# Kernel optimization log

Hardware: AMD Instinct MI355X
Metric: run time of the kernel (lower is better)

The kernel has to match this reference:

```python
import jax, jax.numpy as jnp
import numpy as np

D_MODEL = 192
D_STATE = 16
D_CONV = 3
EXPAND = 2
D_INNER = EXPAND * D_MODEL
DT_RANK = (D_MODEL + 15) // 16  # ceil(d_model/16) = 12


def setup_inputs() -> dict:
    key = jax.random.key(0)
    ks = jax.random.split(key, 8)
    B, H, W = 4, 32, 32
    sc = lambda n: 1.0 / np.sqrt(n)
    x = jax.random.normal(ks[0], (B, H, W, D_MODEL), jnp.float32)
    W_in = jax.random.normal(ks[1], (D_MODEL, 2 * D_INNER), jnp.float32) * sc(D_MODEL)
    conv_w = jax.random.normal(ks[2], (D_INNER, 1, D_CONV, D_CONV), jnp.float32) * sc(D_CONV * D_CONV)
    conv_b = jnp.zeros((D_INNER,), jnp.float32)
    W_x = jax.random.normal(ks[3], (D_INNER, DT_RANK + 2 * D_STATE), jnp.float32) * sc(D_INNER)
    W_dt = jax.random.normal(ks[4], (DT_RANK, D_INNER), jnp.float32) * sc(DT_RANK)
    b_dt = jnp.zeros((D_INNER,), jnp.float32)
    A_log = jnp.log(jnp.tile(jnp.arange(1, D_STATE + 1, dtype=jnp.float32), (D_INNER, 1)))
    D_param = jnp.ones((D_INNER,), jnp.float32)
    W_out = jax.random.normal(ks[5], (D_INNER, D_MODEL), jnp.float32) * sc(D_INNER)
    gamma = jnp.ones((D_INNER,), jnp.float32)
    beta = jnp.zeros((D_INNER,), jnp.float32)
    return {"x": x, "W_in": W_in, "conv_w": conv_w, "conv_b": conv_b,
            "W_x": W_x, "W_dt": W_dt, "b_dt": b_dt, "A_log": A_log,
            "D_param": D_param, "W_out": W_out, "gamma": gamma, "beta": beta}


def _ssm_scan(u, W_x, W_dt, b_dt, A_log, D_param):
    # u: (B, L, D_inner). Log-cumsum closed-form linear SSM scan.
    x_dbl = u @ W_x                                   # (B,L,dt_rank+2N)
    dt = x_dbl[..., :DT_RANK]
    B_mat = x_dbl[..., DT_RANK:DT_RANK + D_STATE]     # (B,L,N)
    C_mat = x_dbl[..., DT_RANK + D_STATE:]            # (B,L,N)
    dt = jax.nn.softplus(dt @ W_dt + b_dt)            # (B,L,D)
    A = -jnp.exp(A_log)                               # (D,N)
    log_dA = jnp.einsum('bld,dn->bldn', dt, A)        # (B,L,D,N)
    dB_u = jnp.einsum('bld,bln->bldn', dt, B_mat) * u[..., None]
    log_decay = jnp.cumsum(log_dA, axis=1)
    decay = jnp.exp(log_decay)
    h = decay * jnp.cumsum(dB_u / (decay + 1e-12), axis=1)
    y = jnp.einsum('bldn,bln->bld', h, C_mat)
    return y + u * D_param


def reference(x, W_in, conv_w, conv_b, W_x, W_dt, b_dt, A_log, D_param, W_out, gamma, beta):
    B, H, W, C = x.shape
    xz = x @ W_in                                     # (B,H,W,2*D_inner)
    x_val, z = xz[..., :D_INNER], xz[..., D_INNER:]
    # depthwise 3x3 conv in NCHW
    xc = jnp.transpose(x_val, (0, 3, 1, 2))
    xc = jax.lax.conv_general_dilated(
        xc, conv_w, window_strides=(1, 1), padding='SAME',
        feature_group_count=D_INNER,
        dimension_numbers=('NCHW', 'OIHW', 'NCHW'))
    xc = xc + conv_b[None, :, None, None]
    xc = jax.nn.silu(xc)
    xv = jnp.transpose(xc, (0, 2, 3, 1))              # (B,H,W,D_inner)

    scan = lambda u: _ssm_scan(u, W_x, W_dt, b_dt, A_log, D_param)
    s1 = xv.reshape(B, H * W, D_INNER)                # row-major
    s2 = s1[:, ::-1]
    s3 = jnp.transpose(xv, (0, 2, 1, 3)).reshape(B, W * H, D_INNER)  # column-major
    s4 = s3[:, ::-1]
    y1 = scan(s1)
    y2 = scan(s2)[:, ::-1]
    y3 = scan(s3)
    y4 = scan(s4)[:, ::-1]
    # map column-major scans back to row-major order
    y3 = jnp.transpose(y3.reshape(B, W, H, D_INNER), (0, 2, 1, 3)).reshape(B, H * W, D_INNER)
    y4 = jnp.transpose(y4.reshape(B, W, H, D_INNER), (0, 2, 1, 3)).reshape(B, H * W, D_INNER)
    y = y1 + y2 + y3 + y4

    # LayerNorm over last dim (eps=1e-5)
    mu = jnp.mean(y, axis=-1, keepdims=True)
    var = jnp.mean(jnp.square(y - mu), axis=-1, keepdims=True)
    y = (y - mu) * jax.lax.rsqrt(var + 1e-5) * gamma + beta

    y = y.reshape(B, H, W, D_INNER) * jax.nn.silu(z)
    return y @ W_out
```

## Files before the change

kernel.cpp:

```cpp
#include <hip/hip_runtime.h>
#include <hip/hip_fp16.h>

#define DMODEL 192
#define DINNER 384
#define NPOS   4096
#define SEQL   1024
#define DSTATE 16
#define DTRANK 12
#define TILE   32

__device__ __forceinline__ float silu_f(float v) { return v * (1.f / (1.f + __expf(-v))); }

__device__ __forceinline__ int scan_pos(int dir, int l) {
    int s = (dir & 1) ? (SEQL - 1 - l) : l;
    return (dir & 2) ? (((s & 31) << 5) | (s >> 5)) : s;
}

template<int CTRL>
__device__ __forceinline__ float dpp_mov(float v) {
    return __int_as_float(__builtin_amdgcn_update_dpp(
        0, __float_as_int(v), CTRL, 0xF, 0xF, true));
}

__global__ void k1_inproj(const float* __restrict__ x, const float* __restrict__ W_in,
                          float* __restrict__ x_val, float* __restrict__ gz) {
    const int t = threadIdx.x;
    const int bi = blockIdx.x;
    const int colg = bi % 3;
    const int pos0 = (bi / 3) << 3;
    const int col = colg * 256 + t;

    const float* xr = x + pos0 * DMODEL;

    float acc[8] = {0,0,0,0,0,0,0,0};
    for (int c = 0; c < DMODEL; c += 4) {
        float w0 = W_in[(c + 0) * 768 + col];
        float w1 = W_in[(c + 1) * 768 + col];
        float w2 = W_in[(c + 2) * 768 + col];
        float w3 = W_in[(c + 3) * 768 + col];
#pragma unroll
        for (int g = 0; g < 8; ++g) {
            const float4 xv = *(const float4*)&xr[g * DMODEL + c];
            acc[g] += xv.x * w0 + xv.y * w1 + xv.z * w2 + xv.w * w3;
        }
    }
    if (col < DINNER) {
#pragma unroll
        for (int g = 0; g < 8; ++g) x_val[(pos0 + g) * DINNER + col] = acc[g];
    } else {
#pragma unroll
        for (int g = 0; g < 8; ++g) gz[(pos0 + g) * DINNER + (col - DINNER)] = silu_f(acc[g]);
    }
}

__global__ void k2_conv_dt(const float* __restrict__ x_val,
                           const float* __restrict__ conv_w, const float* __restrict__ conv_b,
                           const float* __restrict__ W_x, const float* __restrict__ W_dt,
                           const float* __restrict__ b_dt, const float* __restrict__ Dp,
                           __half* __restrict__ u_out, float* __restrict__ xd_out,
                           float* __restrict__ dt32, float* __restrict__ y_acc) {
    __shared__ float us[DINNER];
    __shared__ float part[8 * 44];
    __shared__ float xdl[44];
    const int t = threadIdx.x;
    const int pos = blockIdx.x;
    const int b = pos >> 10, hw = pos & 1023, h = hw >> 5, w = hw & 31;

    float acc = conv_b[t];
#pragma unroll
    for (int i = 0; i < 3; ++i) {
        int hh = h + i - 1;
        if (hh < 0 || hh > 31) continue;
#pragma unroll
        for (int j = 0; j < 3; ++j) {
            int ww = w + j - 1;
            if (ww < 0 || ww > 31) continue;
            acc += x_val[((b * 32 + hh) * 32 + ww) * DINNER + t] * conv_w[t * 9 + i * 3 + j];
        }
    }
    float uv = silu_f(acc);
    us[t] = uv;
    u_out[pos * DINNER + t] = __float2half(uv);
    __syncthreads();

    if (t < 352) {
        int o = t % 44, p = t / 44;
        float s = 0.f;
        int j0 = p * 48;
        for (int j = j0; j < j0 + 48; ++j) s += us[j] * W_x[j * 44 + o];
        part[p * 44 + o] = s;
    }
    __syncthreads();
    if (t < 44) {
        float s = 0.f;
#pragma unroll
        for (int p = 0; p < 8; ++p) s += part[p * 44 + t];
        int o;
        if (t < DTRANK)               o = t;
        else if (t < DTRANK + DSTATE) o = DTRANK + 2 * (t - DTRANK);
        else                          o = DTRANK + 1 + 2 * (t - DTRANK - DSTATE);
        xd_out[pos * 48 + o] = s;
        xdl[t] = s;
    }
    __syncthreads();

    float raw = b_dt[t];
#pragma unroll
    for (int r = 0; r < DTRANK; ++r) raw += xdl[r] * W_dt[r * DINNER + t];
    dt32[pos * DINNER + t] = fmaxf(raw, 0.f) + log1pf(__expf(-fabsf(raw)));

    y_acc[pos * DINNER + t] = 4.f * Dp[t] * uv;
}

__device__ __forceinline__ void gll16(const void* g, void* l) {
    __builtin_amdgcn_global_load_lds(
        (const __attribute__((address_space(1))) void*)g,
        (__attribute__((address_space(3))) void*)l, 16, 0, 0);
}

__device__ __forceinline__ void k3_stage(int l0, int dir, int d0, int wv, int lane,
                                         const float* __restrict__ dtb,
                                         const float* __restrict__ xb,
                                         const __half* __restrict__ ub,
                                         float* dt_d, float* bc_d, __half* u_d) {
    if (wv == 0) {
#pragma unroll
        for (int s = 0; s < 2; ++s) {
            int j = s * 16 + (lane >> 2);
            int pos = scan_pos(dir, l0 + j);
            gll16(dtb + pos * DINNER + d0 + (lane & 3) * 4, dt_d + s * 16 * 16);
        }
    } else if (wv == 3) {
        int pos = scan_pos(dir, l0 + (lane >> 1));
        gll16((const char*)ub + (size_t)(pos * DINNER + d0) * 2 + (lane & 1) * 16, u_d);
    } else {
        int jb0 = (wv - 1) * 16;
#pragma unroll
        for (int s = 0; s < 2; ++s) {
            int jb = jb0 + s * 8;
            int pos = scan_pos(dir, l0 + jb + (lane >> 3));
            gll16(xb + pos * 48 + DTRANK + (lane & 7) * 4, bc_d + jb * 32);
        }
    }
}

__device__ __forceinline__ bool k3_chunk(float A, float& cum, float& S,
                                         const float* __restrict__ dt_s,
                                         const float* __restrict__ bc_s,
                                         const __half* __restrict__ u_s,
                                         int jb, int l0, int dir, int dl, int n,
                                         float* __restrict__ yb, int d) {
    float dtv[8], Bv[8], Cv[8], uv[8];
#pragma unroll
    for (int k = 0; k < 8; ++k) {
        dtv[k] = dt_s[(jb + k) * 16 + dl];
        Bv[k]  = bc_s[(jb + k) * 32 + 2 * n];
        Cv[k]  = bc_s[(jb + k) * 32 + 2 * n + 1];
        uv[k]  = __half2float(u_s[(jb + k) * 16 + dl]);
    }
    float decay[8];
#pragma unroll
    for (int k = 0; k < 8; ++k) { cum += dtv[k] * A; decay[k] = __builtin_amdgcn_exp2f(cum); }
    float rc[8];
#pragma unroll
    for (int k = 0; k < 8; ++k) rc[k] = __builtin_amdgcn_rcpf(decay[k] + 1e-12f);
    float c[8];
#pragma unroll
    for (int k = 0; k < 8; ++k) {
        S += (dtv[k] * Bv[k] * uv[k]) * rc[k];
        c[k] = decay[k] * S * Cv[k];
    }
#pragma unroll
    for (int k = 0; k < 8; ++k) {
        float v = c[k];
        v += dpp_mov<0xB1>(v);
        v += dpp_mov<0x4E>(v);
        v += dpp_mov<0x124>(v);
        v += dpp_mov<0x128>(v);
        c[k] = v;
    }
    if (n == 0) {
#pragma unroll
        for (int k = 0; k < 8; ++k) {
            int pos = scan_pos(dir, l0 + jb + k);
            atomicAdd(&yb[pos * DINNER + d], c[k]);
        }
    }
    return __ballot(cum > -158.7f) != 0ull;
}

__global__ void __launch_bounds__(256, 1)
k3_scan(const __half* __restrict__ u, const float* __restrict__ xd,
        const float* __restrict__ dt32, const float* __restrict__ A_log,
        float* __restrict__ y_acc) {
    __shared__ float  dt_s[2][TILE * 16];
    __shared__ float  BC_s[2][TILE * 32];
    __shared__ __half u_s [2][TILE * 16];
    __shared__ int    alive_w[2][4];

    const int t = threadIdx.x;
    const int lane = t & 63, wv = t >> 6;
    const int n = t & 15, dl = t >> 4;
    const int bi = blockIdx.x;
    const int chunk = bi % 24;
    const int b = (bi / 24) % 4;
    const int dir = bi / 96;
    const int d0 = chunk * 16, d = d0 + dl;

    const float A = -__expf(A_log[d * DSTATE + n]) * 1.4426950408889634f;

    const __half* ub  = u    + b * SEQL * DINNER;
    const float* xb   = xd   + b * SEQL * 48;
    const float* dtb  = dt32 + b * SEQL * DINNER;
    float* yb = y_acc + b * SEQL * DINNER;

    k3_stage(0, dir, d0, wv, lane, dtb, xb, ub, dt_s[0], BC_s[0], u_s[0]);
    __syncthreads();

    float cum = 0.f, S = 0.f;
    bool alive = true;
    int buf = 0, par = 0;
    for (int l0 = 0; l0 < SEQL; l0 += TILE) {
        const int ln = (l0 + TILE < SEQL) ? (l0 + TILE) : l0;
        k3_stage(ln, dir, d0, wv, lane, dtb, xb, ub,
                 dt_s[buf ^ 1], BC_s[buf ^ 1], u_s[buf ^ 1]);
        if (alive) {
#pragma unroll
            for (int jb = 0; jb < TILE; jb += 8) {
                alive = k3_chunk(A, cum, S, dt_s[buf], BC_s[buf], u_s[buf],
                                 jb, l0, dir, dl, n, yb, d);
                if (!alive) break;
            }
        }
        if (lane == 0) alive_w[par][wv] = alive ? 1 : 0;
        __syncthreads();
        const int any = alive_w[par][0] | alive_w[par][1] | alive_w[par][2] | alive_w[par][3];
        buf ^= 1; par ^= 1;
        if (!any) return;
    }
}

__global__ void k4_out(const float* __restrict__ y_acc, const float* __restrict__ gz,
                       const float* __restrict__ gamma, const float* __restrict__ beta,
                       const float* __restrict__ W_out, float* __restrict__ out) {
    __shared__ float g_s[8 * DINNER];
    __shared__ float red[12];
    const int t = threadIdx.x;
    const int half = t / 192, tc = t % 192;
    const int lane = t & 63, wv = t >> 6;
    const int pos0 = blockIdx.x << 3;

    const float g0c = gamma[tc], g1c = gamma[tc + 192];
    const float b0c = beta[tc],  b1c = beta[tc + 192];

    for (int it = 0; it < 4; ++it) {
        int p = it * 2 + half;
        int pos = pos0 + p;
        float y0 = y_acc[pos * DINNER + tc];
        float y1 = y_acc[pos * DINNER + tc + 192];

        float s = y0 + y1;
#pragma unroll
        for (int off = 32; off > 0; off >>= 1) s += __shfl_xor(s, off);
        if (lane == 0) red[wv] = s;
        __syncthreads();
        float mu = (red[half * 3] + red[half * 3 + 1] + red[half * 3 + 2]) * (1.f / 384.f);

        float d0 = y0 - mu, d1 = y1 - mu;
        float sq = d0 * d0 + d1 * d1;
#pragma unroll
        for (int off = 32; off > 0; off >>= 1) sq += __shfl_xor(sq, off);
        if (lane == 0) red[6 + wv] = sq;
        __syncthreads();
        float var = (red[6 + half * 3] + red[6 + half * 3 + 1] + red[6 + half * 3 + 2]) * (1.f / 384.f);
        float inv = rsqrtf(var + 1e-5f);

        g_s[p * DINNER + tc]       = (d0 * inv * g0c + b0c) * gz[pos * DINNER + tc];
        g_s[p * DINNER + tc + 192] = (d1 * inv * g1c + b1c) * gz[pos * DINNER + tc + 192];
    }
    __syncthreads();

    float acc[4] = {0.f, 0.f, 0.f, 0.f};
    const int pbase = half * 4;
    for (int dd = 0; dd < DINNER; dd += 4) {
        float w0 = W_out[(dd + 0) * DMODEL + tc];
        float w1 = W_out[(dd + 1) * DMODEL + tc];
        float w2 = W_out[(dd + 2) * DMODEL + tc];
        float w3 = W_out[(dd + 3) * DMODEL + tc];
#pragma unroll
        for (int i = 0; i < 4; ++i) {
            const float4 g = *(const float4*)&g_s[(pbase + i) * DINNER + dd];
            acc[i] += g.x * w0 + g.y * w1 + g.z * w2 + g.w * w3;
        }
    }
#pragma unroll
    for (int i = 0; i < 4; ++i) out[(pos0 + pbase + i) * DMODEL + tc] = acc[i];
}

extern "C" void kernel_launch(void* const* d_in, const int* in_sizes, int n_in,
                              void* d_out, int out_size, void* d_ws, size_t ws_size,
                              hipStream_t stream) {
    (void)in_sizes; (void)n_in; (void)out_size; (void)ws_size;
    const float* x      = (const float*)d_in[0];
    const float* W_in   = (const float*)d_in[1];
    const float* conv_w = (const float*)d_in[2];
    const float* conv_b = (const float*)d_in[3];
    const float* W_x    = (const float*)d_in[4];
    const float* W_dt   = (const float*)d_in[5];
    const float* b_dt   = (const float*)d_in[6];
    const float* A_log  = (const float*)d_in[7];
    const float* Dp     = (const float*)d_in[8];
    const float* W_out  = (const float*)d_in[9];
    const float* gamma  = (const float*)d_in[10];
    const float* beta   = (const float*)d_in[11];

    char* base = (char*)d_ws;
    float*  x_val = (float*)base;
    __half* u     = (__half*)(base + 6291456);
    float*  xd    = (float*)(base + 9437184);
    float*  dt32  = (float*)(base + 10223616);
    float*  gz    = (float*)(base + 16515072);
    float*  y_acc = (float*)(base + 22806528);

    hipLaunchKernelGGL(k1_inproj, dim3(NPOS / 8 * 3), dim3(256), 0, stream, x, W_in, x_val, gz);
    hipLaunchKernelGGL(k2_conv_dt, dim3(NPOS), dim3(384), 0, stream,
                       x_val, conv_w, conv_b, W_x, W_dt, b_dt, Dp, u, xd, dt32, y_acc);
    hipLaunchKernelGGL(k3_scan, dim3(384), dim3(256), 0, stream,
                       u, xd, dt32, A_log, y_acc);
    hipLaunchKernelGGL(k4_out, dim3(NPOS / 8), dim3(384), 0, stream,
                       y_acc, gz, gamma, beta, W_out, (float*)d_out);
}
```

Before: 203.7 us.

## Split SSM scan into segmented three-pass chunked scan across more blocks

The sequential scan over 1024 positions per (dir,batch,channel-chunk) block is replaced by three kernels. The first computes per-32-step dt partial sums. The second computes each 128-step segment's local state contribution. The third combines prefix decay and prior segment states, then rescans its segment to emit outputs. This raises the block count from 384 to 3072 to fill the GPU and shorten the serial critical path. The cost is two extra launches, extra global traffic, and each segment being scanned twice.

```diff
diff --git a/kernel.cpp b/kernel.cpp
--- a/kernel.cpp
+++ b/kernel.cpp
@@ -8,6 +8,9 @@
 #define DSTATE 16
 #define DTRANK 12
 #define TILE   32
+#define NSEG   8
+#define SEGL   128
+#define NFINE  32
 
 __device__ __forceinline__ float silu_f(float v) { return v * (1.f / (1.f + __expf(-v))); }
 
@@ -189,54 +192,177 @@
     return __ballot(cum > -158.7f) != 0ull;
 }
 
+__global__ void k3a_dtsum(const float* __restrict__ dt32, float* __restrict__ dtsum) {
+    const int t = threadIdx.x;
+    const int bi = blockIdx.x;
+    const int f = bi & 31;
+    const int b = (bi >> 5) & 3;
+    const int ord = bi >> 7;
+    const float* dtb = dt32 + b * SEQL * DINNER;
+    float s = 0.f;
+#pragma unroll 4
+    for (int j = 0; j < 32; ++j) {
+        int sidx = f * 32 + j;
+        int pos = ord ? (((sidx & 31) << 5) | (sidx >> 5)) : sidx;
+        s += dtb[pos * DINNER + t];
+    }
+    dtsum[((ord * 4 + b) * NFINE + f) * DINNER + t] = s;
+}
+
+__device__ __forceinline__ float k3_cum_in(const float* __restrict__ dtsum,
+                                           int dir, int b, int g, int d, float A) {
+    const float* dts = dtsum + ((dir >> 1) * 4 + b) * NFINE * DINNER;
+    float p0 = 0.f, p1 = 0.f, p2 = 0.f, p3 = 0.f;
+    const int fpmax = 4 * g;
+    for (int fp = 0; fp < fpmax; fp += 4) {
+        int h0 = (dir & 1) ? (NFINE - 1 - (fp + 0)) : (fp + 0);
+        int h1 = (dir & 1) ? (NFINE - 1 - (fp + 1)) : (fp + 1);
+        int h2 = (dir & 1) ? (NFINE - 1 - (fp + 2)) : (fp + 2);
+        int h3 = (dir & 1) ? (NFINE - 1 - (fp + 3)) : (fp + 3);
+        p0 += dts[h0 * DINNER + d];
+        p1 += dts[h1 * DINNER + d];
+        p2 += dts[h2 * DINNER + d];
+        p3 += dts[h3 * DINNER + d];
+    }
+    return A * ((p0 + p1) + (p2 + p3));
+}
+
 __global__ void __launch_bounds__(256, 1)
-k3_scan(const __half* __restrict__ u, const float* __restrict__ xd,
+k3b_sseg(const __half* __restrict__ u, const float* __restrict__ xd,
+         const float* __restrict__ dt32, const float* __restrict__ A_log,
+         const float* __restrict__ dtsum, float* __restrict__ S_seg) {
+    __shared__ float  dt_s[2][TILE * 16];
+    __shared__ float  BC_s[2][TILE * 32];
+    __shared__ __half u_s [2][TILE * 16];
+    __shared__ int    vote[4];
+
+    const int t = threadIdx.x;
+    const int lane = t & 63, wv = t >> 6;
+    const int n = t & 15, dl = t >> 4;
+    const int bi = blockIdx.x;
+    const int g = bi & 7;
+    const int r = bi >> 3;
+    const int chunk = r % 24;
+    const int r2 = r / 24;
+    const int b = r2 & 3, dir = r2 >> 2;
+    const int d0 = chunk * 16, d = d0 + dl;
+
+    const float A = -__expf(A_log[d * DSTATE + n]) * 1.4426950408889634f;
+    float cum = k3_cum_in(dtsum, dir, b, g, d, A);
+
+    bool alive = (__ballot(cum > -158.7f) != 0ull);
+    if (lane == 0) vote[wv] = alive ? 1 : 0;
+    __syncthreads();
+    float* Sout = S_seg + bi * 256 + t;
+    if (!(vote[0] | vote[1] | vote[2] | vote[3])) { *Sout = 0.f; return; }
+
+    const __half* ub  = u    + b * SEQL * DINNER;
+    const float* xb   = xd   + b * SEQL * 48;
+    const float* dtb  = dt32 + b * SEQL * DINNER;
+
+    const int l0 = g * SEGL;
+    k3_stage(l0, dir, d0, wv, lane, dtb, xb, ub, dt_s[0], BC_s[0], u_s[0]);
+    __syncthreads();
+
+    float S = 0.f;
+    int buf = 0;
+    for (int tt = 0; tt < SEGL / TILE; ++tt) {
+        const int lc = l0 + tt * TILE;
+        const int ln = (tt < SEGL / TILE - 1) ? (lc + TILE) : lc;
+        k3_stage(ln, dir, d0, wv, lane, dtb, xb, ub,
+                 dt_s[buf ^ 1], BC_s[buf ^ 1], u_s[buf ^ 1]);
+        if (alive) {
+#pragma unroll
+            for (int jb = 0; jb < TILE; jb += 8) {
+                float dtv[8], Bv[8], uv[8];
+#pragma unroll
+                for (int k = 0; k < 8; ++k) {
+                    dtv[k] = dt_s[buf][(jb + k) * 16 + dl];
+                    Bv[k]  = BC_s[buf][(jb + k) * 32 + 2 * n];
+                    uv[k]  = __half2float(u_s[buf][(jb + k) * 16 + dl]);
+                }
+                float decay[8];
+#pragma unroll
+                for (int k = 0; k < 8; ++k) { cum += dtv[k] * A; decay[k] = __builtin_amdgcn_exp2f(cum); }
+                float rc[8];
+#pragma unroll
+                for (int k = 0; k < 8; ++k) rc[k] = __builtin_amdgcn_rcpf(decay[k] + 1e-12f);
+#pragma unroll
+                for (int k = 0; k < 8; ++k) S += (dtv[k] * Bv[k] * uv[k]) * rc[k];
+                alive = (__ballot(cum > -158.7f) != 0ull);
+                if (!alive) break;
+            }
+        }
+        __syncthreads();
+        buf ^= 1;
+    }
+    *Sout = S;
+}
+
+__global__ void __launch_bounds__(256, 1)
+k3c_out(const __half* __restrict__ u, const float* __restrict__ xd,
         const float* __restrict__ dt32, const float* __restrict__ A_log,
+        const float* __restrict__ dtsum, const float* __restrict__ S_seg,
         float* __restrict__ y_acc) {
     __shared__ float  dt_s[2][TILE * 16];
     __shared__ float  BC_s[2][TILE * 32];
     __shared__ __half u_s [2][TILE * 16];
-    __shared__ int    alive_w[2][4];
+    __shared__ int    vote[4];
 
     const int t = threadIdx.x;
     const int lane = t & 63, wv = t >> 6;
     const int n = t & 15, dl = t >> 4;
     const int bi = blockIdx.x;
-    const int chunk = bi % 24;
-    const int b = (bi / 24) % 4;
-    const int dir = bi / 96;
+    const int g = bi & 7;
+    const int r = bi >> 3;
+    const int chunk = r % 24;
+    const int r2 = r / 24;
+    const int b = r2 & 3, dir = r2 >> 2;
     const int d0 = chunk * 16, d = d0 + dl;
 
     const float A = -__expf(A_log[d * DSTATE + n]) * 1.4426950408889634f;
+    float cum = k3_cum_in(dtsum, dir, b, g, d, A);
+
+    bool alive = (__ballot(cum > -158.7f) != 0ull);
+    if (lane == 0) vote[wv] = alive ? 1 : 0;
+    __syncthreads();
+    if (!(vote[0] | vote[1] | vote[2] | vote[3])) return;
+
+    float S;
+    {
+        const float* Sp = S_seg + (size_t)(bi - g) * 256 + t;
+        float s0 = 0.f, s1 = 0.f;
+        int gp = 0;
+        for (; gp + 1 < g; gp += 2) { s0 += Sp[gp * 256]; s1 += Sp[(gp + 1) * 256]; }
+        if (gp < g) s0 += Sp[gp * 256];
+        S = s0 + s1;
+    }
 
     const __half* ub  = u    + b * SEQL * DINNER;
     const float* xb   = xd   + b * SEQL * 48;
     const float* dtb  = dt32 + b * SEQL * DINNER;
     float* yb = y_acc + b * SEQL * DINNER;
 
-    k3_stage(0, dir, d0, wv, lane, dtb, xb, ub, dt_s[0], BC_s[0], u_s[0]);
-    __syncthreads();
-
-    float cum = 0.f, S = 0.f;
-    bool alive = true;
-    int buf = 0, par = 0;
-    for (int l0 = 0; l0 < SEQL; l0 += TILE) {
-        const int ln = (l0 + TILE < SEQL) ? (l0 + TILE) : l0;
+    const int l0 = g * SEGL;
+    k3_stage(l0, dir, d0, wv, lane, dtb, xb, ub, dt_s[0], BC_s[0], u_s[0]);
+    __syncthreads();
+
+    int buf = 0;
+    for (int tt = 0; tt < SEGL / TILE; ++tt) {
+        const int lc = l0 + tt * TILE;
+        const int ln = (tt < SEGL / TILE - 1) ? (lc + TILE) : lc;
         k3_stage(ln, dir, d0, wv, lane, dtb, xb, ub,
                  dt_s[buf ^ 1], BC_s[buf ^ 1], u_s[buf ^ 1]);
         if (alive) {
 #pragma unroll
             for (int jb = 0; jb < TILE; jb += 8) {
                 alive = k3_chunk(A, cum, S, dt_s[buf], BC_s[buf], u_s[buf],
-                                 jb, l0, dir, dl, n, yb, d);
+                                 jb, lc, dir, dl, n, yb, d);
                 if (!alive) break;
             }
         }
-        if (lane == 0) alive_w[par][wv] = alive ? 1 : 0;
         __syncthreads();
-        const int any = alive_w[par][0] | alive_w[par][1] | alive_w[par][2] | alive_w[par][3];
-        buf ^= 1; par ^= 1;
-        if (!any) return;
+        buf ^= 1;
     }
 }
 
@@ -321,12 +447,17 @@
     float*  dt32  = (float*)(base + 10223616);
     float*  gz    = (float*)(base + 16515072);
     float*  y_acc = (float*)(base + 22806528);
+    float*  dtsum = (float*)(base + 29097984);
+    float*  S_seg = (float*)(base + 29491200);
 
     hipLaunchKernelGGL(k1_inproj, dim3(NPOS / 8 * 3), dim3(256), 0, stream, x, W_in, x_val, gz);
     hipLaunchKernelGGL(k2_conv_dt, dim3(NPOS), dim3(384), 0, stream,
                        x_val, conv_w, conv_b, W_x, W_dt, b_dt, Dp, u, xd, dt32, y_acc);
-    hipLaunchKernelGGL(k3_scan, dim3(384), dim3(256), 0, stream,
-                       u, xd, dt32, A_log, y_acc);
+    hipLaunchKernelGGL(k3a_dtsum, dim3(256), dim3(384), 0, stream, dt32, dtsum);
+    hipLaunchKernelGGL(k3b_sseg, dim3(4 * 4 * 24 * NSEG), dim3(256), 0, stream,
+                       u, xd, dt32, A_log, dtsum, S_seg);
+    hipLaunchKernelGGL(k3c_out, dim3(4 * 4 * 24 * NSEG), dim3(256), 0, stream,
+                       u, xd, dt32, A_log, dtsum, S_seg, y_acc);
     hipLaunchKernelGGL(k4_out, dim3(NPOS / 8), dim3(384), 0, stream,
                        y_acc, gz, gamma, beta, W_out, (float*)d_out);
 }
```

New measurement: 283.6 us. 1.39x slower.

## Process two channel groups per scan thread to halve scan blocks and share B/C loads

Applied to the files above, without the earlier changes.

The scan kernel now assigns 32 channels per block instead of 16, so each thread runs two independent recurrences (A and B) interleaved, with single-channel fallbacks once one of them dies out. B/C staging is shared across twice as many channels, and the two chains give more instruction-level parallelism. The grid shrinks from 384 to 192 blocks. This lowers occupancy and parallelism on a chip with many CUs, and raises register pressure.

```diff
diff --git a/kernel.cpp b/kernel.cpp
--- a/kernel.cpp
+++ b/kernel.cpp
@@ -125,14 +125,17 @@
                                          float* dt_d, float* bc_d, __half* u_d) {
     if (wv == 0) {
 #pragma unroll
+        for (int s = 0; s < 4; ++s) {
+            int pos = scan_pos(dir, l0 + s * 8 + (lane >> 3));
+            gll16(dtb + pos * DINNER + d0 + (lane & 7) * 4, dt_d + s * 8 * 32);
+        }
+    } else if (wv == 3) {
+#pragma unroll
         for (int s = 0; s < 2; ++s) {
-            int j = s * 16 + (lane >> 2);
-            int pos = scan_pos(dir, l0 + j);
-            gll16(dtb + pos * DINNER + d0 + (lane & 3) * 4, dt_d + s * 16 * 16);
-        }
-    } else if (wv == 3) {
-        int pos = scan_pos(dir, l0 + (lane >> 1));
-        gll16((const char*)ub + (size_t)(pos * DINNER + d0) * 2 + (lane & 1) * 16, u_d);
+            int pos = scan_pos(dir, l0 + s * 16 + (lane >> 2));
+            gll16((const char*)ub + (size_t)(pos * DINNER + d0) * 2 + (lane & 3) * 16,
+                  u_d + s * 16 * 32);
+        }
     } else {
         int jb0 = (wv - 1) * 16;
 #pragma unroll
@@ -144,19 +147,20 @@
     }
 }
 
-__device__ __forceinline__ bool k3_chunk(float A, float& cum, float& S,
-                                         const float* __restrict__ dt_s,
-                                         const float* __restrict__ bc_s,
-                                         const __half* __restrict__ u_s,
-                                         int jb, int l0, int dir, int dl, int n,
-                                         float* __restrict__ yb, int d) {
+__device__ __forceinline__ bool k3_chunk1(float A, float& cum, float& S,
+                                          const float* __restrict__ dt_s,
+                                          const float* __restrict__ bc_s,
+                                          const __half* __restrict__ u_s,
+                                          int jb, int l0, int dir, int dl, int n,
+                                          float* __restrict__ yb, int d, int coff) {
     float dtv[8], Bv[8], Cv[8], uv[8];
 #pragma unroll
     for (int k = 0; k < 8; ++k) {
-        dtv[k] = dt_s[(jb + k) * 16 + dl];
-        Bv[k]  = bc_s[(jb + k) * 32 + 2 * n];
-        Cv[k]  = bc_s[(jb + k) * 32 + 2 * n + 1];
-        uv[k]  = __half2float(u_s[(jb + k) * 16 + dl]);
+        int row = (jb + k) * 32;
+        dtv[k] = dt_s[row + coff + dl];
+        Bv[k]  = bc_s[row + 2 * n];
+        Cv[k]  = bc_s[row + 2 * n + 1];
+        uv[k]  = __half2float(u_s[row + coff + dl]);
     }
     float decay[8];
 #pragma unroll
@@ -189,25 +193,87 @@
     return __ballot(cum > -158.7f) != 0ull;
 }
 
+__device__ __forceinline__ void k3_chunk2(float AA, float AB,
+                                          float& cumA, float& cumB,
+                                          float& SA, float& SB,
+                                          const float* __restrict__ dt_s,
+                                          const float* __restrict__ bc_s,
+                                          const __half* __restrict__ u_s,
+                                          int jb, int l0, int dir, int dl, int n,
+                                          float* __restrict__ yb, int d0,
+                                          bool& aliveA, bool& aliveB) {
+    float dtvA[8], dtvB[8], Bv[8], Cv[8], uvA[8], uvB[8];
+#pragma unroll
+    for (int k = 0; k < 8; ++k) {
+        int row = (jb + k) * 32;
+        dtvA[k] = dt_s[row + dl];
+        dtvB[k] = dt_s[row + 16 + dl];
+        Bv[k]   = bc_s[row + 2 * n];
+        Cv[k]   = bc_s[row + 2 * n + 1];
+        uvA[k]  = __half2float(u_s[row + dl]);
+        uvB[k]  = __half2float(u_s[row + 16 + dl]);
+    }
+    float decA[8], decB[8];
+#pragma unroll
+    for (int k = 0; k < 8; ++k) {
+        cumA += dtvA[k] * AA; decA[k] = __builtin_amdgcn_exp2f(cumA);
+        cumB += dtvB[k] * AB; decB[k] = __builtin_amdgcn_exp2f(cumB);
+    }
+    float rcA[8], rcB[8];
+#pragma unroll
+    for (int k = 0; k < 8; ++k) {
+        rcA[k] = __builtin_amdgcn_rcpf(decA[k] + 1e-12f);
+        rcB[k] = __builtin_amdgcn_rcpf(decB[k] + 1e-12f);
+    }
+    float cA[8], cB[8];
+#pragma unroll
+    for (int k = 0; k < 8; ++k) {
+        SA += (dtvA[k] * Bv[k] * uvA[k]) * rcA[k];
+        cA[k] = decA[k] * SA * Cv[k];
+        SB += (dtvB[k] * Bv[k] * uvB[k]) * rcB[k];
+        cB[k] = decB[k] * SB * Cv[k];
+    }
+#pragma unroll
+    for (int k = 0; k < 8; ++k) {
+        float vA = cA[k], vB = cB[k];
+        vA += dpp_mov<0xB1>(vA);   vB += dpp_mov<0xB1>(vB);
+        vA += dpp_mov<0x4E>(vA);   vB += dpp_mov<0x4E>(vB);
+        vA += dpp_mov<0x124>(vA);  vB += dpp_mov<0x124>(vB);
+        vA += dpp_mov<0x128>(vA);  vB += dpp_mov<0x128>(vB);
+        cA[k] = vA; cB[k] = vB;
+    }
+    if (n == 0) {
+#pragma unroll
+        for (int k = 0; k < 8; ++k) {
+            int pos = scan_pos(dir, l0 + jb + k);
+            atomicAdd(&yb[pos * DINNER + d0 + dl], cA[k]);
+            atomicAdd(&yb[pos * DINNER + d0 + 16 + dl], cB[k]);
+        }
+    }
+    aliveA = __ballot(cumA > -158.7f) != 0ull;
+    aliveB = __ballot(cumB > -158.7f) != 0ull;
+}
+
 __global__ void __launch_bounds__(256, 1)
 k3_scan(const __half* __restrict__ u, const float* __restrict__ xd,
         const float* __restrict__ dt32, const float* __restrict__ A_log,
         float* __restrict__ y_acc) {
-    __shared__ float  dt_s[2][TILE * 16];
+    __shared__ float  dt_s[2][TILE * 32];
     __shared__ float  BC_s[2][TILE * 32];
-    __shared__ __half u_s [2][TILE * 16];
+    __shared__ __half u_s [2][TILE * 32];
     __shared__ int    alive_w[2][4];
 
     const int t = threadIdx.x;
     const int lane = t & 63, wv = t >> 6;
     const int n = t & 15, dl = t >> 4;
     const int bi = blockIdx.x;
-    const int chunk = bi % 24;
-    const int b = (bi / 24) % 4;
-    const int dir = bi / 96;
-    const int d0 = chunk * 16, d = d0 + dl;
-
-    const float A = -__expf(A_log[d * DSTATE + n]) * 1.4426950408889634f;
+    const int cp = bi % 12;
+    const int b = (bi / 12) % 4;
+    const int dir = bi / 48;
+    const int d0 = cp * 32;
+
+    const float AA = -__expf(A_log[(d0 + dl) * DSTATE + n])      * 1.4426950408889634f;
+    const float AB = -__expf(A_log[(d0 + 16 + dl) * DSTATE + n]) * 1.4426950408889634f;
 
     const __half* ub  = u    + b * SEQL * DINNER;
     const float* xb   = xd   + b * SEQL * 48;
@@ -217,22 +283,31 @@
     k3_stage(0, dir, d0, wv, lane, dtb, xb, ub, dt_s[0], BC_s[0], u_s[0]);
     __syncthreads();
 
-    float cum = 0.f, S = 0.f;
-    bool alive = true;
+    float cumA = 0.f, SA = 0.f, cumB = 0.f, SB = 0.f;
+    bool aliveA = true, aliveB = true;
     int buf = 0, par = 0;
     for (int l0 = 0; l0 < SEQL; l0 += TILE) {
         const int ln = (l0 + TILE < SEQL) ? (l0 + TILE) : l0;
         k3_stage(ln, dir, d0, wv, lane, dtb, xb, ub,
                  dt_s[buf ^ 1], BC_s[buf ^ 1], u_s[buf ^ 1]);
-        if (alive) {
+        if (aliveA | aliveB) {
 #pragma unroll
             for (int jb = 0; jb < TILE; jb += 8) {
-                alive = k3_chunk(A, cum, S, dt_s[buf], BC_s[buf], u_s[buf],
-                                 jb, l0, dir, dl, n, yb, d);
-                if (!alive) break;
+                if (aliveA & aliveB) {
+                    k3_chunk2(AA, AB, cumA, cumB, SA, SB,
+                              dt_s[buf], BC_s[buf], u_s[buf],
+                              jb, l0, dir, dl, n, yb, d0, aliveA, aliveB);
+                } else if (aliveA) {
+                    aliveA = k3_chunk1(AA, cumA, SA, dt_s[buf], BC_s[buf], u_s[buf],
+                                       jb, l0, dir, dl, n, yb, d0 + dl, 0);
+                } else {
+                    aliveB = k3_chunk1(AB, cumB, SB, dt_s[buf], BC_s[buf], u_s[buf],
+                                       jb, l0, dir, dl, n, yb, d0 + 16 + dl, 16);
+                }
+                if (!(aliveA | aliveB)) break;
             }
         }
-        if (lane == 0) alive_w[par][wv] = alive ? 1 : 0;
+        if (lane == 0) alive_w[par][wv] = (aliveA | aliveB) ? 1 : 0;
         __syncthreads();
         const int any = alive_w[par][0] | alive_w[par][1] | alive_w[par][2] | alive_w[par][3];
         buf ^= 1; par ^= 1;
@@ -325,7 +400,7 @@
     hipLaunchKernelGGL(k1_inproj, dim3(NPOS / 8 * 3), dim3(256), 0, stream, x, W_in, x_val, gz);
     hipLaunchKernelGGL(k2_conv_dt, dim3(NPOS), dim3(384), 0, stream,
                        x_val, conv_w, conv_b, W_x, W_dt, b_dt, Dp, u, xd, dt32, y_acc);
-    hipLaunchKernelGGL(k3_scan, dim3(384), dim3(256), 0, stream,
+    hipLaunchKernelGGL(k3_scan, dim3(192), dim3(256), 0, stream,
                        u, xd, dt32, A_log, y_acc);
     hipLaunchKernelGGL(k4_out, dim3(NPOS / 8), dim3(384), 0, stream,
                        y_acc, gz, gamma, beta, W_out, (float*)d_out);
```

Result: slower. 215.4 us (+5.8%).

## Split scan sequence into four parallel segments with two-pass carry propagation

Applied to the files above, without the earlier changes.

The sequential scan over 1024 positions is split into four 256-long segments, each handled by 256 threads of a 1024-thread block. A first lean pass computes each segment's partial dB*u/decay sum, and per-segment dt prefix sums give the starting log-decay. A second pass then recomputes the outputs with the carried-in state. This shortens the serial dependency chain by about four times, at the cost of roughly double the arithmetic, extra LDS use and block-wide syncs.

```diff
diff --git a/kernel.cpp b/kernel.cpp
--- a/kernel.cpp
+++ b/kernel.cpp
@@ -8,6 +8,8 @@
 #define DSTATE 16
 #define DTRANK 12
 #define TILE   32
+#define NSEG   4
+#define SEGL   256
 
 __device__ __forceinline__ float silu_f(float v) { return v * (1.f / (1.f + __expf(-v))); }
 
@@ -118,23 +120,23 @@
         (__attribute__((address_space(3))) void*)l, 16, 0, 0);
 }
 
-__device__ __forceinline__ void k3_stage(int l0, int dir, int d0, int wv, int lane,
+__device__ __forceinline__ void k3_stage(int l0, int dir, int d0, int wrole, int lane,
                                          const float* __restrict__ dtb,
                                          const float* __restrict__ xb,
                                          const __half* __restrict__ ub,
                                          float* dt_d, float* bc_d, __half* u_d) {
-    if (wv == 0) {
+    if (wrole == 0) {
 #pragma unroll
         for (int s = 0; s < 2; ++s) {
             int j = s * 16 + (lane >> 2);
             int pos = scan_pos(dir, l0 + j);
             gll16(dtb + pos * DINNER + d0 + (lane & 3) * 4, dt_d + s * 16 * 16);
         }
-    } else if (wv == 3) {
+    } else if (wrole == 3) {
         int pos = scan_pos(dir, l0 + (lane >> 1));
         gll16((const char*)ub + (size_t)(pos * DINNER + d0) * 2 + (lane & 1) * 16, u_d);
     } else {
-        int jb0 = (wv - 1) * 16;
+        int jb0 = (wrole - 1) * 16;
 #pragma unroll
         for (int s = 0; s < 2; ++s) {
             int jb = jb0 + s * 8;
@@ -142,6 +144,29 @@
             gll16(xb + pos * 48 + DTRANK + (lane & 7) * 4, bc_d + jb * 32);
         }
     }
+}
+
+__device__ __forceinline__ bool k3_chunk_lean(float A, float& cum, float& S,
+                                              const float* __restrict__ dt_s,
+                                              const float* __restrict__ bc_s,
+                                              const __half* __restrict__ u_s,
+                                              int jb, int dl, int n) {
+    float dtv[8], Bv[8], uv[8];
+#pragma unroll
+    for (int k = 0; k < 8; ++k) {
+        dtv[k] = dt_s[(jb + k) * 16 + dl];
+        Bv[k]  = bc_s[(jb + k) * 32 + 2 * n];
+        uv[k]  = __half2float(u_s[(jb + k) * 16 + dl]);
+    }
+    float decay[8];
+#pragma unroll
+    for (int k = 0; k < 8; ++k) { cum += dtv[k] * A; decay[k] = __builtin_amdgcn_exp2f(cum); }
+    float rc[8];
+#pragma unroll
+    for (int k = 0; k < 8; ++k) rc[k] = __builtin_amdgcn_rcpf(decay[k] + 1e-12f);
+#pragma unroll
+    for (int k = 0; k < 8; ++k) S += (dtv[k] * Bv[k] * uv[k]) * rc[k];
+    return __ballot(cum > -158.7f) != 0ull;
 }
 
 __device__ __forceinline__ bool k3_chunk(float A, float& cum, float& S,
@@ -189,18 +214,24 @@
     return __ballot(cum > -158.7f) != 0ull;
 }
 
-__global__ void __launch_bounds__(256, 1)
-k3_scan(const __half* __restrict__ u, const float* __restrict__ xd,
-        const float* __restrict__ dt32, const float* __restrict__ A_log,
-        float* __restrict__ y_acc) {
-    __shared__ float  dt_s[2][TILE * 16];
-    __shared__ float  BC_s[2][TILE * 32];
-    __shared__ __half u_s [2][TILE * 16];
-    __shared__ int    alive_w[2][4];
+__global__ void __launch_bounds__(1024, 4)
+k3_fused(const __half* __restrict__ u, const float* __restrict__ xd,
+         const float* __restrict__ dt32, const float* __restrict__ A_log,
+         float* __restrict__ y_acc) {
+    __shared__ float  dt_s[NSEG][2][TILE * 16];
+    __shared__ float  BC_s[NSEG][2][TILE * 32];
+    __shared__ __half u_s [NSEG][2][TILE * 16];
+    __shared__ float  SA[NSEG * 256];
+    __shared__ float  segdt[NSEG * 16];
+    __shared__ int    vote[2][16];
 
     const int t = threadIdx.x;
-    const int lane = t & 63, wv = t >> 6;
-    const int n = t & 15, dl = t >> 4;
+    const int lane = t & 63;
+    const int wv16 = t >> 6;
+    const int wrole = wv16 & 3;
+    const int seg = t >> 8;
+    const int tid = t & 255;
+    const int dl = tid >> 4, n = t & 15;
     const int bi = blockIdx.x;
     const int chunk = bi % 24;
     const int b = (bi / 24) % 4;
@@ -214,27 +245,83 @@
     const float* dtb  = dt32 + b * SEQL * DINNER;
     float* yb = y_acc + b * SEQL * DINNER;
 
-    k3_stage(0, dir, d0, wv, lane, dtb, xb, ub, dt_s[0], BC_s[0], u_s[0]);
-    __syncthreads();
-
-    float cum = 0.f, S = 0.f;
-    bool alive = true;
+    k3_stage(seg * SEGL, dir, d0, wrole, lane, dtb, xb, ub,
+             dt_s[seg][0], BC_s[seg][0], u_s[seg][0]);
+
+    {
+        float dtp = 0.f;
+#pragma unroll
+        for (int j = 0; j < 16; ++j) {
+            int pos = scan_pos(dir, seg * SEGL + n + 16 * j);
+            dtp += dtb[pos * DINNER + d];
+        }
+        dtp += dpp_mov<0xB1>(dtp);
+        dtp += dpp_mov<0x4E>(dtp);
+        dtp += dpp_mov<0x124>(dtp);
+        dtp += dpp_mov<0x128>(dtp);
+        if (n == 0) segdt[seg * 16 + dl] = dtp;
+    }
+    __syncthreads();
+
+    float pre = 0.f;
+    for (int g2 = 0; g2 < seg; ++g2) pre += segdt[g2 * 16 + dl];
+    const float cum_in = A * pre;
+
+    float cum = cum_in, S = 0.f;
+    bool alive = (__ballot(cum_in > -158.7f) != 0ull);
     int buf = 0, par = 0;
-    for (int l0 = 0; l0 < SEQL; l0 += TILE) {
-        const int ln = (l0 + TILE < SEQL) ? (l0 + TILE) : l0;
-        k3_stage(ln, dir, d0, wv, lane, dtb, xb, ub,
-                 dt_s[buf ^ 1], BC_s[buf ^ 1], u_s[buf ^ 1]);
+    for (int tt = 0; tt < SEGL / TILE; ++tt) {
+        const int tn = (tt < SEGL / TILE - 1) ? (tt + 1) : tt;
+        k3_stage(seg * SEGL + tn * TILE, dir, d0, wrole, lane, dtb, xb, ub,
+                 dt_s[seg][buf ^ 1], BC_s[seg][buf ^ 1], u_s[seg][buf ^ 1]);
         if (alive) {
 #pragma unroll
             for (int jb = 0; jb < TILE; jb += 8) {
-                alive = k3_chunk(A, cum, S, dt_s[buf], BC_s[buf], u_s[buf],
-                                 jb, l0, dir, dl, n, yb, d);
+                alive = k3_chunk_lean(A, cum, S, dt_s[seg][buf], BC_s[seg][buf],
+                                      u_s[seg][buf], jb, dl, n);
                 if (!alive) break;
             }
         }
-        if (lane == 0) alive_w[par][wv] = alive ? 1 : 0;
+        if (lane == 0) vote[par][wv16] = alive ? 1 : 0;
         __syncthreads();
-        const int any = alive_w[par][0] | alive_w[par][1] | alive_w[par][2] | alive_w[par][3];
+        const int4* vp = (const int4*)vote[par];
+        int4 a0 = vp[0], a1 = vp[1], a2 = vp[2], a3 = vp[3];
+        int any = a0.x | a0.y | a0.z | a0.w | a1.x | a1.y | a1.z | a1.w |
+                  a2.x | a2.y | a2.z | a2.w | a3.x | a3.y | a3.z | a3.w;
+        buf ^= 1; par ^= 1;
+        if (!any) break;
+    }
+    SA[seg * 256 + tid] = S;
+
+    k3_stage(seg * SEGL, dir, d0, wrole, lane, dtb, xb, ub,
+             dt_s[seg][buf ^ 1], BC_s[seg][buf ^ 1], u_s[seg][buf ^ 1]);
+    __syncthreads();
+    buf ^= 1;
+
+    float Sb = 0.f;
+    for (int g2 = 0; g2 < seg; ++g2) Sb += SA[g2 * 256 + tid];
+    cum = cum_in;
+    alive = (__ballot(cum_in > -158.7f) != 0ull);
+
+    for (int tt = 0; tt < SEGL / TILE; ++tt) {
+        const int lc = seg * SEGL + tt * TILE;
+        const int tn = (tt < SEGL / TILE - 1) ? (tt + 1) : tt;
+        k3_stage(seg * SEGL + tn * TILE, dir, d0, wrole, lane, dtb, xb, ub,
+                 dt_s[seg][buf ^ 1], BC_s[seg][buf ^ 1], u_s[seg][buf ^ 1]);
+        if (alive) {
+#pragma unroll
+            for (int jb = 0; jb < TILE; jb += 8) {
+                alive = k3_chunk(A, cum, Sb, dt_s[seg][buf], BC_s[seg][buf],
+                                 u_s[seg][buf], jb, lc, dir, dl, n, yb, d);
+                if (!alive) break;
+            }
+        }
+        if (lane == 0) vote[par][wv16] = alive ? 1 : 0;
+        __syncthreads();
+        const int4* vp = (const int4*)vote[par];
+        int4 a0 = vp[0], a1 = vp[1], a2 = vp[2], a3 = vp[3];
+        int any = a0.x | a0.y | a0.z | a0.w | a1.x | a1.y | a1.z | a1.w |
+                  a2.x | a2.y | a2.z | a2.w | a3.x | a3.y | a3.z | a3.w;
         buf ^= 1; par ^= 1;
         if (!any) return;
     }
@@ -325,7 +412,7 @@
     hipLaunchKernelGGL(k1_inproj, dim3(NPOS / 8 * 3), dim3(256), 0, stream, x, W_in, x_val, gz);
     hipLaunchKernelGGL(k2_conv_dt, dim3(NPOS), dim3(384), 0, stream,
                        x_val, conv_w, conv_b, W_x, W_dt, b_dt, Dp, u, xd, dt32, y_acc);
-    hipLaunchKernelGGL(k3_scan, dim3(384), dim3(256), 0, stream,
+    hipLaunchKernelGGL(k3_fused, dim3(384), dim3(1024), 0, stream,
                        u, xd, dt32, A_log, y_acc);
     hipLaunchKernelGGL(k4_out, dim3(NPOS / 8), dim3(384), 0, stream,
                        y_acc, gz, gamma, beta, W_out, (float*)d_out);
```

After: 251.1 us. +23.3%, slower.
